# Kernel tuning notes

Hardware: AMD Instinct MI355X
Metric: run time of the kernel (lower is better)

Reference implementation:

```python
import jax, jax.numpy as jnp
import numpy as np

B, D, E, H, O, TOPK = 16384, 256, 8, 128, 1, 2
THRESHOLD = 0.5
NUM_SCALES = 3
TAUS = np.linspace(5.0, 20.0, NUM_SCALES)  # MSLIFNeuron tau_range=(5,20), num_scales=3


def setup_inputs() -> dict:
    key = jax.random.key(0)
    ks = jax.random.split(key, 10)
    s = lambda fan: 1.0 / np.sqrt(fan)
    return {
        "features": jax.random.normal(ks[0], (B, D), jnp.float32),
        "Wg": jax.random.normal(ks[1], (D, E), jnp.float32) * s(D),
        "W1": jax.random.normal(ks[2], (E, D, H), jnp.float32) * s(D),
        "b1": jnp.zeros((E, H), jnp.float32),
        "Wp": jax.random.normal(ks[3], (E, H, H), jnp.float32) * s(H),
        "bp": jnp.zeros((E, H), jnp.float32),
        "mix_logit": jnp.zeros((E,), jnp.float32),
        "Wo": jax.random.normal(ks[4], (E, H, O), jnp.float32) * s(H),
        "bo": jnp.zeros((E, O), jnp.float32),
    }


def _mslif_spikes(x):
    # multi-scale LIF, single step from zero state: v_s = x * (1 - exp(-dt/tau_s))
    decays = jnp.asarray(1.0 - np.exp(-1.0 / TAUS), x.dtype)  # [S]
    v = x[:, None, :] * decays[None, :, None]                  # [B,S,D]
    return (v > THRESHOLD).astype(x.dtype).mean(axis=1)        # [B,D]


def reference(features, Wg, W1, b1, Wp, bp, mix_logit, Wo, bo):
    # gating: softmax over experts, top-k renormalized
    gate = jax.nn.softmax(features @ Wg, axis=-1)              # [B,E]
    _, idx = jax.lax.top_k(gate, TOPK)                         # [B,K]
    mask = jax.nn.one_hot(idx, E, dtype=gate.dtype).sum(1)     # [B,E]
    w = gate * mask
    w = w / (w.sum(-1, keepdims=True) + 1e-10)

    # spike generator (computed in expert forward; not used downstream)
    _spikes = _mslif_spikes(features)

    # NeuroDynArch expert: static core + plasticity mix
    core = jax.nn.relu(jnp.einsum('bd,edh->beh', features, W1) + b1[None])
    plast = jnp.tanh(jnp.einsum('beh,ehk->bek', core, Wp) + bp[None])
    mix = jax.nn.sigmoid(mix_logit)[None, :, None]             # [1,E,1]
    mixed = core * (1.0 - mix) + plast * mix                   # [B,E,H]
    out_e = jnp.einsum('beh,eho->beo', mixed, Wo) + bo[None]   # [B,E,O]
    return jnp.einsum('beo,be->bo', out_e, w)                  # [B,O]
```

## Files before the change

kernel.cpp:

```cpp
#include <hip/hip_runtime.h>

#define BB 16384
#define DD 256
#define EE 8
#define HH 128

typedef __attribute__((ext_vector_type(8))) short short8;
typedef __attribute__((ext_vector_type(4))) float f32x4;

__device__ __forceinline__ ushort f2bf(float f){
    const unsigned u = __float_as_uint(f);
    return (ushort)((u + 0x7fffu + ((u >> 16) & 1u)) >> 16);
}
__device__ __forceinline__ float bf2f(ushort s){
    return __uint_as_float(((unsigned)s) << 16);
}
__device__ __forceinline__ float fast_tanh(float v){
    v = fminf(fmaxf(v, -15.0f), 15.0f);
    const float a = __expf(2.0f * v);
    return (a - 1.0f) / (a + 1.0f);
}

__global__ __launch_bounds__(256) void transpose_kernel(
    const float* __restrict__ W1, const float* __restrict__ Wp,
    ushort* __restrict__ W1t, ushort* __restrict__ Wpt)
{
    __shared__ float tile[64 * 68];
    int b = blockIdx.x;
    const float* src; ushort* dst; int K;
    int k0, h0;
    if (b < 64){
        const int e = b >> 3, kt = (b >> 1) & 3, ht = b & 1;
        src = W1 + (size_t)e * DD * HH;  dst = W1t + (size_t)e * HH * DD;
        K = DD; k0 = kt * 64; h0 = ht * 64;
    } else {
        b -= 64;
        const int e = b >> 2, kt = (b >> 1) & 1, ht = b & 1;
        src = Wp + (size_t)e * HH * HH;  dst = Wpt + (size_t)e * HH * HH;
        K = HH; k0 = kt * 64; h0 = ht * 64;
    }
    const int t = threadIdx.x;
    #pragma unroll
    for (int j = 0; j < 4; j++){
        const int idx = t + 256 * j;
        const int kk = idx >> 4, hh = (idx & 15) * 4;
        const float4 v = *(const float4*)(src + (size_t)(k0 + kk) * HH + h0 + hh);
        *(float4*)&tile[kk * 68 + hh] = v;
    }
    __syncthreads();
    #pragma unroll
    for (int j = 0; j < 4; j++){
        const int idx = t + 256 * j;
        const int hh = idx >> 4, kk = (idx & 15) * 4;
        ushort4 o;
        o.x = f2bf(tile[(kk + 0) * 68 + hh]);
        o.y = f2bf(tile[(kk + 1) * 68 + hh]);
        o.z = f2bf(tile[(kk + 2) * 68 + hh]);
        o.w = f2bf(tile[(kk + 3) * 68 + hh]);
        *(ushort4*)&dst[(size_t)(h0 + hh) * K + k0 + kk] = o;
    }
}

__global__ __launch_bounds__(256) void routing_kernel(
    const float* __restrict__ x, const float* __restrict__ Wg,
    int* __restrict__ counts, int* __restrict__ rowids, float* __restrict__ wgts)
{
    __shared__ __align__(16) float WgT[EE][DD];
    __shared__ int   le[128];
    __shared__ float lw[128];
    __shared__ int   loff[128];
    __shared__ int   lcount[EE];
    __shared__ int   lbase[EE];

    const int t = threadIdx.x;
    {
        const float4* g = (const float4*)(Wg + t * EE);
        const float4 a = g[0], b = g[1];
        WgT[0][t] = a.x; WgT[1][t] = a.y; WgT[2][t] = a.z; WgT[3][t] = a.w;
        WgT[4][t] = b.x; WgT[5][t] = b.y; WgT[6][t] = b.z; WgT[7][t] = b.w;
    }
    if (t < EE) lcount[t] = 0;
    __syncthreads();

    const int lane = t & 63;
    const int wid  = t >> 6;
    const int rowBase = blockIdx.x * 64;

    for (int it = 0; it < 16; it++){
        const int slot = wid * 16 + it;
        const int row  = rowBase + slot;
        const float4 xv = *(const float4*)(x + row * DD + lane * 4);
        float p[EE];
        #pragma unroll
        for (int e = 0; e < EE; e++){
            const float4 w = *(const float4*)&WgT[e][lane * 4];
            p[e] = xv.x * w.x + xv.y * w.y + xv.z * w.z + xv.w * w.w;
        }
        #pragma unroll
        for (int off = 32; off >= 1; off >>= 1){
            #pragma unroll
            for (int e = 0; e < EE; e++) p[e] += __shfl_down(p[e], off, 64);
        }
        if (lane == 0){
            int e0 = 0; float l0 = p[0];
            #pragma unroll
            for (int e = 1; e < EE; e++){ if (p[e] > l0){ l0 = p[e]; e0 = e; } }
            int e1 = -1; float l1 = -3.0e38f;
            #pragma unroll
            for (int e = 0; e < EE; e++){ if (e != e0 && p[e] > l1){ l1 = p[e]; e1 = e; } }
            const float tt  = __expf(l1 - l0);
            const float inv = 1.0f / (1.0f + tt);
            le[slot]      = e0;  lw[slot]      = inv;
            le[64 + slot] = e1;  lw[64 + slot] = tt * inv;
        }
    }
    __syncthreads();
    if (t < 128) loff[t] = atomicAdd(&lcount[le[t]], 1);
    __syncthreads();
    if (t < EE) lbase[t] = atomicAdd(&counts[t], lcount[t]);
    __syncthreads();
    if (t < 128){
        const int e   = le[t];
        const int pos = lbase[e] + loff[t];
        rowids[e * BB + pos] = rowBase + (t & 63);
        wgts[e * BB + pos]   = lw[t];
    }
}

#define XS_S 264
#define CS_S 136

__global__ __launch_bounds__(256, 2) void expert_kernel(
    const float* __restrict__ x,
    const ushort* __restrict__ W1t, const float* __restrict__ b1,
    const ushort* __restrict__ Wpt, const float* __restrict__ bp,
    const float* __restrict__ mix_logit,
    const float* __restrict__ Wo, const float* __restrict__ bo,
    const int* __restrict__ counts, const int* __restrict__ rowids,
    const float* __restrict__ wgts, float* __restrict__ out)
{
    const int me    = blockIdx.y;
    const int cnt   = counts[me];
    const int start = blockIdx.x * 64;
    if (start >= cnt) return;

    __shared__ ushort Xs[64 * XS_S];
    __shared__ ushort coreS[64 * CS_S];
    __shared__ int   rid_s[64];
    __shared__ float w_s[64];

    const int t = threadIdx.x;
    if (t < 64){
        const int idx = start + t;
        if (idx < cnt){ rid_s[t] = rowids[me * BB + idx]; w_s[t] = wgts[me * BB + idx]; }
        else          { rid_s[t] = 0;                     w_s[t] = 0.0f; }
    }
    __syncthreads();

    #pragma unroll
    for (int j = 0; j < 16; j++){
        const int idx = t + 256 * j;
        const int r  = idx >> 6;
        const int kq = (idx & 63) << 2;
        const float4 v = *(const float4*)(x + (size_t)rid_s[r] * DD + kq);
        ushort4 bv;
        bv.x = f2bf(v.x); bv.y = f2bf(v.y); bv.z = f2bf(v.z); bv.w = f2bf(v.w);
        *(ushort4*)&Xs[r * XS_S + kq] = bv;
    }
    __syncthreads();

    const int lane = t & 63;
    const int w    = t >> 6;
    const int m16  = lane & 15;
    const int q    = lane >> 4;
    const int r0   = 32 * (w >> 1);
    const int c0   = 64 * (w & 1);

    f32x4 acc[2][4];
    #pragma unroll
    for (int ct = 0; ct < 4; ct++){
        const float bj = b1[me * HH + c0 + ct * 16 + m16];
        #pragma unroll
        for (int rt = 0; rt < 2; rt++) acc[rt][ct] = (f32x4){bj, bj, bj, bj};
    }
    const ushort* W1te = W1t + (size_t)me * HH * DD;
    #pragma unroll
    for (int ks = 0; ks < 8; ks++){
        const int k0 = ks * 32;
        short8 af[2], bf[4];
        #pragma unroll
        for (int rt = 0; rt < 2; rt++)
            af[rt] = *(const short8*)&Xs[(r0 + rt * 16 + m16) * XS_S + k0 + q * 8];
        #pragma unroll
        for (int ct = 0; ct < 4; ct++)
            bf[ct] = *(const short8*)&W1te[(size_t)(c0 + ct * 16 + m16) * DD + k0 + q * 8];
        #pragma unroll
        for (int rt = 0; rt < 2; rt++)
            #pragma unroll
            for (int ct = 0; ct < 4; ct++)
                acc[rt][ct] = __builtin_amdgcn_mfma_f32_16x16x32_bf16(af[rt], bf[ct], acc[rt][ct], 0, 0, 0);
    }

    #pragma unroll
    for (int rt = 0; rt < 2; rt++)
        #pragma unroll
        for (int ct = 0; ct < 4; ct++)
            #pragma unroll
            for (int j = 0; j < 4; j++){
                const int row = r0 + rt * 16 + q * 4 + j;
                const int col = c0 + ct * 16 + m16;
                coreS[row * CS_S + col] = f2bf(fmaxf(acc[rt][ct][j], 0.0f));
            }
    __syncthreads();

    #pragma unroll
    for (int ct = 0; ct < 4; ct++){
        const float bj = bp[me * HH + c0 + ct * 16 + m16];
        #pragma unroll
        for (int rt = 0; rt < 2; rt++) acc[rt][ct] = (f32x4){bj, bj, bj, bj};
    }
    const ushort* Wpte = Wpt + (size_t)me * HH * HH;
    #pragma unroll
    for (int ks = 0; ks < 4; ks++){
        const int k0 = ks * 32;
        short8 af[2], bf[4];
        #pragma unroll
        for (int rt = 0; rt < 2; rt++)
            af[rt] = *(const short8*)&coreS[(r0 + rt * 16 + m16) * CS_S + k0 + q * 8];
        #pragma unroll
        for (int ct = 0; ct < 4; ct++)
            bf[ct] = *(const short8*)&Wpte[(size_t)(c0 + ct * 16 + m16) * HH + k0 + q * 8];
        #pragma unroll
        for (int rt = 0; rt < 2; rt++)
            #pragma unroll
            for (int ct = 0; ct < 4; ct++)
                acc[rt][ct] = __builtin_amdgcn_mfma_f32_16x16x32_bf16(af[rt], bf[ct], acc[rt][ct], 0, 0, 0);
    }

    const float mv  = 1.0f / (1.0f + __expf(-mix_logit[me]));
    const float om  = 1.0f - mv;
    const float bov = bo[me];
    float wo[4];
    #pragma unroll
    for (int ct = 0; ct < 4; ct++) wo[ct] = Wo[me * HH + c0 + ct * 16 + m16];

    float red[2][4];
    #pragma unroll
    for (int rt = 0; rt < 2; rt++)
        #pragma unroll
        for (int j = 0; j < 4; j++){
            float s = 0.0f;
            const int row = r0 + rt * 16 + q * 4 + j;
            #pragma unroll
            for (int ct = 0; ct < 4; ct++){
                const int col = c0 + ct * 16 + m16;
                const float pl = fast_tanh(acc[rt][ct][j]);
                const float cv = bf2f(coreS[row * CS_S + col]);
                s = fmaf(om * cv + mv * pl, wo[ct], s);
            }
            red[rt][j] = s;
        }
    #pragma unroll
    for (int off = 8; off >= 1; off >>= 1)
        #pragma unroll
        for (int rt = 0; rt < 2; rt++)
            #pragma unroll
            for (int j = 0; j < 4; j++)
                red[rt][j] += __shfl_xor(red[rt][j], off, 64);

    if (m16 == 0){
        const float bb = (c0 == 0) ? bov : 0.0f;
        #pragma unroll
        for (int rt = 0; rt < 2; rt++)
            #pragma unroll
            for (int j = 0; j < 4; j++){
                const int row = r0 + rt * 16 + q * 4 + j;
                const float ww = w_s[row];
                if (ww != 0.0f) atomicAdd(&out[rid_s[row]], (red[rt][j] + bb) * ww);
            }
    }
}

extern "C" void kernel_launch(void* const* d_in, const int* in_sizes, int n_in,
                              void* d_out, int out_size, void* d_ws, size_t ws_size,
                              hipStream_t stream) {
    (void)in_sizes; (void)n_in; (void)out_size; (void)ws_size;
    const float* x   = (const float*)d_in[0];
    const float* Wg  = (const float*)d_in[1];
    const float* W1  = (const float*)d_in[2];
    const float* b1  = (const float*)d_in[3];
    const float* Wp  = (const float*)d_in[4];
    const float* bp  = (const float*)d_in[5];
    const float* ml  = (const float*)d_in[6];
    const float* Wo  = (const float*)d_in[7];
    const float* bo  = (const float*)d_in[8];
    float* out = (float*)d_out;

    char* ws = (char*)d_ws;
    int*    counts = (int*)ws;
    int*    rowids = (int*)(ws + 256);
    float*  wgts   = (float*)(ws + 256 + (size_t)EE * BB * 4);
    ushort* W1t    = (ushort*)(ws + 256 + 2 * (size_t)EE * BB * 4);
    ushort* Wpt    = W1t + (size_t)EE * HH * DD;

    hipMemsetAsync(counts, 0, EE * sizeof(int), stream);
    hipMemsetAsync(out, 0, BB * sizeof(float), stream);

    transpose_kernel<<<96, 256, 0, stream>>>(W1, Wp, W1t, Wpt);
    routing_kernel<<<BB / 64, 256, 0, stream>>>(x, Wg, counts, rowids, wgts);
    expert_kernel<<<dim3(BB / 64, EE), 256, 0, stream>>>(
        x, W1t, b1, Wpt, bp, ml, Wo, bo, counts, rowids, wgts, out);
}
```

Baseline: 127.2 us.

## Fuse weight transpose, routing and zero-init into one prep kernel

Replaces the two memsets and the separate transpose and routing kernels with a single prep kernel. Its first 96 blocks transpose and convert the weights to bf16, and block 0 also resets the expert counts. The remaining blocks zero the output and route 16 rows each instead of 64, so there are more, smaller blocks. Routing blocks spin on a global flag before adding to the counts; this removes launch and memset overhead. The flag is never cleared between calls, so on later calls the count reset can race with the routing atomics.

Result: slower. 158.3 us (+24.4%).

```diff
diff --git a/kernel.cpp b/kernel.cpp
--- a/kernel.cpp
+++ b/kernel.cpp
@@ -4,6 +4,7 @@
 #define DD 256
 #define EE 8
 #define HH 128
+#define MAGIC 0x13579BDF
 
 typedef __attribute__((ext_vector_type(8))) short short8;
 typedef __attribute__((ext_vector_type(4))) float f32x4;
@@ -21,73 +22,84 @@
     return (a - 1.0f) / (a + 1.0f);
 }
 
-__global__ __launch_bounds__(256) void transpose_kernel(
+__global__ __launch_bounds__(256) void prep_kernel(
     const float* __restrict__ W1, const float* __restrict__ Wp,
-    ushort* __restrict__ W1t, ushort* __restrict__ Wpt)
+    ushort* __restrict__ W1t, ushort* __restrict__ Wpt,
+    const float* __restrict__ x, const float* __restrict__ Wg,
+    int* __restrict__ counts, int* __restrict__ flag,
+    int* __restrict__ rowids, float* __restrict__ wgts, float* __restrict__ out)
 {
     __shared__ float tile[64 * 68];
-    int b = blockIdx.x;
-    const float* src; ushort* dst; int K;
-    int k0, h0;
-    if (b < 64){
-        const int e = b >> 3, kt = (b >> 1) & 3, ht = b & 1;
-        src = W1 + (size_t)e * DD * HH;  dst = W1t + (size_t)e * HH * DD;
-        K = DD; k0 = kt * 64; h0 = ht * 64;
-    } else {
-        b -= 64;
-        const int e = b >> 2, kt = (b >> 1) & 1, ht = b & 1;
-        src = Wp + (size_t)e * HH * HH;  dst = Wpt + (size_t)e * HH * HH;
-        K = HH; k0 = kt * 64; h0 = ht * 64;
-    }
-    const int t = threadIdx.x;
-    #pragma unroll
-    for (int j = 0; j < 4; j++){
-        const int idx = t + 256 * j;
-        const int kk = idx >> 4, hh = (idx & 15) * 4;
-        const float4 v = *(const float4*)(src + (size_t)(k0 + kk) * HH + h0 + hh);
-        *(float4*)&tile[kk * 68 + hh] = v;
-    }
-    __syncthreads();
-    #pragma unroll
-    for (int j = 0; j < 4; j++){
-        const int idx = t + 256 * j;
-        const int hh = idx >> 4, kk = (idx & 15) * 4;
-        ushort4 o;
-        o.x = f2bf(tile[(kk + 0) * 68 + hh]);
-        o.y = f2bf(tile[(kk + 1) * 68 + hh]);
-        o.z = f2bf(tile[(kk + 2) * 68 + hh]);
-        o.w = f2bf(tile[(kk + 3) * 68 + hh]);
-        *(ushort4*)&dst[(size_t)(h0 + hh) * K + k0 + kk] = o;
-    }
-}
-
-__global__ __launch_bounds__(256) void routing_kernel(
-    const float* __restrict__ x, const float* __restrict__ Wg,
-    int* __restrict__ counts, int* __restrict__ rowids, float* __restrict__ wgts)
-{
     __shared__ __align__(16) float WgT[EE][DD];
-    __shared__ int   le[128];
-    __shared__ float lw[128];
-    __shared__ int   loff[128];
+    __shared__ int   le[32];
+    __shared__ float lw[32];
+    __shared__ int   loff[32];
     __shared__ int   lcount[EE];
     __shared__ int   lbase[EE];
 
     const int t = threadIdx.x;
+
+    if (blockIdx.x < 96){
+        int b = blockIdx.x;
+        if (b == 0){
+            if (t < EE) atomicExch(&counts[t], 0);
+            __syncthreads();
+            if (t == 0){
+                __threadfence();
+                __hip_atomic_store(flag, MAGIC, __ATOMIC_RELEASE, __HIP_MEMORY_SCOPE_AGENT);
+            }
+        }
+        const float* src; ushort* dst; int K;
+        int k0, h0;
+        if (b < 64){
+            const int e = b >> 3, kt = (b >> 1) & 3, ht = b & 1;
+            src = W1 + (size_t)e * DD * HH;  dst = W1t + (size_t)e * HH * DD;
+            K = DD; k0 = kt * 64; h0 = ht * 64;
+        } else {
+            b -= 64;
+            const int e = b >> 2, kt = (b >> 1) & 1, ht = b & 1;
+            src = Wp + (size_t)e * HH * HH;  dst = Wpt + (size_t)e * HH * HH;
+            K = HH; k0 = kt * 64; h0 = ht * 64;
+        }
+        #pragma unroll
+        for (int j = 0; j < 4; j++){
+            const int idx = t + 256 * j;
+            const int kk = idx >> 4, hh = (idx & 15) * 4;
+            const float4 v = *(const float4*)(src + (size_t)(k0 + kk) * HH + h0 + hh);
+            *(float4*)&tile[kk * 68 + hh] = v;
+        }
+        __syncthreads();
+        #pragma unroll
+        for (int j = 0; j < 4; j++){
+            const int idx = t + 256 * j;
+            const int hh = idx >> 4, kk = (idx & 15) * 4;
+            ushort4 o;
+            o.x = f2bf(tile[(kk + 0) * 68 + hh]);
+            o.y = f2bf(tile[(kk + 1) * 68 + hh]);
+            o.z = f2bf(tile[(kk + 2) * 68 + hh]);
+            o.w = f2bf(tile[(kk + 3) * 68 + hh]);
+            *(ushort4*)&dst[(size_t)(h0 + hh) * K + k0 + kk] = o;
+        }
+        return;
+    }
+
+    const int rb = blockIdx.x - 96;
+    const int rowBase = rb * 16;
+    if (t < 16) out[rowBase + t] = 0.0f;
     {
         const float4* g = (const float4*)(Wg + t * EE);
-        const float4 a = g[0], b = g[1];
-        WgT[0][t] = a.x; WgT[1][t] = a.y; WgT[2][t] = a.z; WgT[3][t] = a.w;
-        WgT[4][t] = b.x; WgT[5][t] = b.y; WgT[6][t] = b.z; WgT[7][t] = b.w;
+        const float4 a = g[0], b2 = g[1];
+        WgT[0][t] = a.x;  WgT[1][t] = a.y;  WgT[2][t] = a.z;  WgT[3][t] = a.w;
+        WgT[4][t] = b2.x; WgT[5][t] = b2.y; WgT[6][t] = b2.z; WgT[7][t] = b2.w;
     }
     if (t < EE) lcount[t] = 0;
     __syncthreads();
 
     const int lane = t & 63;
     const int wid  = t >> 6;
-    const int rowBase = blockIdx.x * 64;
-
-    for (int it = 0; it < 16; it++){
-        const int slot = wid * 16 + it;
+
+    for (int it = 0; it < 4; it++){
+        const int slot = wid * 4 + it;
         const int row  = rowBase + slot;
         const float4 xv = *(const float4*)(x + row * DD + lane * 4);
         float p[EE];
@@ -111,18 +123,22 @@
             const float tt  = __expf(l1 - l0);
             const float inv = 1.0f / (1.0f + tt);
             le[slot]      = e0;  lw[slot]      = inv;
-            le[64 + slot] = e1;  lw[64 + slot] = tt * inv;
-        }
-    }
-    __syncthreads();
-    if (t < 128) loff[t] = atomicAdd(&lcount[le[t]], 1);
+            le[16 + slot] = e1;  lw[16 + slot] = tt * inv;
+        }
+    }
+    __syncthreads();
+    if (t < 32) loff[t] = atomicAdd(&lcount[le[t]], 1);
+    if (t == 0){
+        while (__hip_atomic_load(flag, __ATOMIC_ACQUIRE, __HIP_MEMORY_SCOPE_AGENT) != MAGIC)
+            __builtin_amdgcn_s_sleep(1);
+    }
     __syncthreads();
     if (t < EE) lbase[t] = atomicAdd(&counts[t], lcount[t]);
     __syncthreads();
-    if (t < 128){
+    if (t < 32){
         const int e   = le[t];
         const int pos = lbase[e] + loff[t];
-        rowids[e * BB + pos] = rowBase + (t & 63);
+        rowids[e * BB + pos] = rowBase + (t & 15);
         wgts[e * BB + pos]   = lw[t];
     }
 }
@@ -298,16 +314,14 @@
 
     char* ws = (char*)d_ws;
     int*    counts = (int*)ws;
+    int*    flag   = (int*)(ws + 64);
     int*    rowids = (int*)(ws + 256);
     float*  wgts   = (float*)(ws + 256 + (size_t)EE * BB * 4);
     ushort* W1t    = (ushort*)(ws + 256 + 2 * (size_t)EE * BB * 4);
     ushort* Wpt    = W1t + (size_t)EE * HH * DD;
 
-    hipMemsetAsync(counts, 0, EE * sizeof(int), stream);
-    hipMemsetAsync(out, 0, BB * sizeof(float), stream);
-
-    transpose_kernel<<<96, 256, 0, stream>>>(W1, Wp, W1t, Wpt);
-    routing_kernel<<<BB / 64, 256, 0, stream>>>(x, Wg, counts, rowids, wgts);
+    prep_kernel<<<96 + BB / 16, 256, 0, stream>>>(
+        W1, Wp, W1t, Wpt, x, Wg, counts, flag, rowids, wgts, out);
     expert_kernel<<<dim3(BB / 64, EE), 256, 0, stream>>>(
         x, W1t, b1, Wpt, bp, ml, Wo, bo, counts, rowids, wgts, out);
 }
```
